# Kernel tuning notes

Hardware: AMD Instinct MI355X
Metric: run time of the kernel (lower is better)

## Reference

```python
import jax, jax.numpy as jnp
from jax import lax
import numpy as np

B, C, H, W = 8, 64, 56, 56
LM = 9              # level_map: NSCT subbands per channel
D = LM * C + C      # 640: swin block dim
DEPTH = 2
WIN = 7
HEADS = 8
KS = 5              # NSCT filter kernel size


def _nsct_filters():
    # fixed nonsubsampled 9-band filter bank (lowpass + 8 directional), stand-in for myNSCTd
    r = np.arange(KS) - KS // 2
    yy, xx = np.meshgrid(r, r, indexing='ij')
    g = np.exp(-(xx ** 2 + yy ** 2) / 4.0)
    g = g / g.sum()
    f = [g]
    for k in range(LM - 1):
        th = k * np.pi / (LM - 1)
        d = (np.cos(th) * xx + np.sin(th) * yy) * g
        d = d - d.mean()
        d = d / np.sqrt((d ** 2).sum())
        f.append(d)
    return jnp.asarray(np.stack(f), dtype=jnp.float32)  # [LM,KS,KS]


def _ct(x):
    # per-(b,c) NSCT decomposition -> [B, LM*C, H, W], band-major (matches transpose(0,2,1,3,4).reshape)
    Bx, Cx, Hx, Wx = x.shape
    K = _nsct_filters()
    k = jnp.tile(K, (Cx, 1, 1))[:, None]  # [Cx*LM,1,KS,KS], out channel index c*LM+band
    o = lax.conv_general_dilated(x, k, (1, 1), 'SAME',
                                 dimension_numbers=('NCHW', 'OIHW', 'NCHW'),
                                 feature_group_count=Cx)
    o = o.reshape(Bx, Cx, LM, Hx, Wx).transpose(0, 2, 1, 3, 4).reshape(Bx, LM * Cx, Hx, Wx)
    return o


def _ict(y):
    # inverse transform: reshape(B,LM,C,H,W).permute(0,2,1,3,4), reconstruct per channel
    Bx = y.shape[0]
    t = y.reshape(Bx, LM, C, H, W).transpose(0, 2, 1, 3, 4).reshape(Bx, C * LM, H, W)
    K = _nsct_filters()
    g = jnp.broadcast_to(K, (C, LM, KS, KS))  # groups=C: 9 subbands -> 1 channel each
    return lax.conv_general_dilated(t, g, (1, 1), 'SAME',
                                    dimension_numbers=('NCHW', 'OIHW', 'NCHW'),
                                    feature_group_count=C)


def _ln(x, g, b):
    m = x.mean(-1, keepdims=True)
    v = x.var(-1, keepdims=True)
    return (x - m) / jnp.sqrt(v + 1e-5) * g + b


def _attn_mask(shift):
    # standard SW-MSA mask for shifted windows
    img = np.zeros((H, W), np.int32)
    c = 0
    for hs in (slice(0, -WIN), slice(-WIN, -shift), slice(-shift, None)):
        for ws in (slice(0, -WIN), slice(-WIN, -shift), slice(-shift, None)):
            img[hs, ws] = c
            c += 1
    a = img.reshape(H // WIN, WIN, W // WIN, WIN).transpose(0, 2, 1, 3).reshape(-1, WIN * WIN)
    m = np.where(a[:, :, None] != a[:, None, :], -1e9, 0.0).astype(np.float32)
    return jnp.asarray(m)  # [nWindows, T, T]


def _swin_block(x, p, shift):
    Bx = x.shape[0]
    T = WIN * WIN
    dh = D // HEADS
    nH, nWw = H // WIN, W // WIN
    sc = x
    h = _ln(x, p['ln1_g'], p['ln1_b'])
    if shift:
        h = jnp.roll(h, (-shift, -shift), (1, 2))
    w = h.reshape(Bx, nH, WIN, nWw, WIN, D).transpose(0, 1, 3, 2, 4, 5).reshape(Bx * nH * nWw, T, D)
    qkv = w @ p['qkv_w'] + p['qkv_b']
    q, k, v = jnp.split(qkv, 3, axis=-1)
    heads = lambda t: t.reshape(-1, T, HEADS, dh).transpose(0, 2, 1, 3)
    q, k, v = heads(q), heads(k), heads(v)
    s = jnp.einsum('nhtd,nhsd->nhts', q, k) / jnp.sqrt(jnp.asarray(dh, x.dtype))
    if shift:
        m = _attn_mask(shift)
        s = (s.reshape(Bx, nH * nWw, HEADS, T, T) + m[None, :, None]).reshape(-1, HEADS, T, T)
    a = jax.nn.softmax(s, -1)
    o = jnp.einsum('nhts,nhsd->nhtd', a, v).transpose(0, 2, 1, 3).reshape(-1, T, D)
    o = o @ p['proj_w'] + p['proj_b']
    o = o.reshape(Bx, nH, nWw, WIN, WIN, D).transpose(0, 1, 3, 2, 4, 5).reshape(Bx, H, W, D)
    if shift:
        o = jnp.roll(o, (shift, shift), (1, 2))
    x = sc + o
    h2 = _ln(x, p['ln2_g'], p['ln2_b'])
    h2 = jax.nn.gelu(h2 @ p['fc1_w'] + p['fc1_b']) @ p['fc2_w'] + p['fc2_b']
    return x + h2


def setup_inputs() -> dict:
    key = jax.random.key(0)
    ks = jax.random.split(key, 8)
    s = 0.02
    n = lambda k, shp: jax.random.normal(k, shp, jnp.float32) * s
    return {
        'x': jax.random.normal(ks[0], (B, C, H, W), jnp.float32),
        'ln1_g': jnp.ones((DEPTH, D), jnp.float32), 'ln1_b': jnp.zeros((DEPTH, D), jnp.float32),
        'qkv_w': n(ks[1], (DEPTH, D, 3 * D)), 'qkv_b': jnp.zeros((DEPTH, 3 * D), jnp.float32),
        'proj_w': n(ks[2], (DEPTH, D, D)), 'proj_b': jnp.zeros((DEPTH, D), jnp.float32),
        'ln2_g': jnp.ones((DEPTH, D), jnp.float32), 'ln2_b': jnp.zeros((DEPTH, D), jnp.float32),
        'fc1_w': n(ks[3], (DEPTH, D, 4 * D)), 'fc1_b': jnp.zeros((DEPTH, 4 * D), jnp.float32),
        'fc2_w': n(ks[4], (DEPTH, 4 * D, D)), 'fc2_b': jnp.zeros((DEPTH, D), jnp.float32),
        'lin_w': n(ks[5], (D, LM * C)), 'lin_b': jnp.zeros((LM * C,), jnp.float32),
        'conv_w': n(ks[6], (C, D)), 'conv_b': jnp.zeros((C,), jnp.float32),
    }


def reference(x, ln1_g, ln1_b, qkv_w, qkv_b, proj_w, proj_b, ln2_g, ln2_b,
              fc1_w, fc1_b, fc2_w, fc2_b, lin_w, lin_b, conv_w, conv_b):
    x2 = jax.nn.relu(x)
    x_trans = lax.stop_gradient(_ct(x2))          # CT detaches its input in the original
    x3 = jnp.concatenate([x_trans, x2], axis=1)   # [B, 10C, H, W]
    x3 = x3.transpose(0, 2, 3, 1)                 # BHWC
    for i in range(DEPTH):
        p = dict(ln1_g=ln1_g[i], ln1_b=ln1_b[i], qkv_w=qkv_w[i], qkv_b=qkv_b[i],
                 proj_w=proj_w[i], proj_b=proj_b[i], ln2_g=ln2_g[i], ln2_b=ln2_b[i],
                 fc1_w=fc1_w[i], fc1_b=fc1_b[i], fc2_w=fc2_w[i], fc2_b=fc2_b[i])
        x3 = _swin_block(x3, p, 0 if i % 2 == 0 else WIN // 2)
    x3 = x3 @ lin_w + lin_b                        # D -> LM*C
    y = x3.transpose(0, 3, 1, 2)                   # [B, 9C, H, W]
    y_trans = lax.stop_gradient(_ict(y))           # ICT detaches its input in the original
    yc = jnp.concatenate([y_trans, y], axis=1)     # [B, 10C, H, W]
    out = jnp.einsum('bchw,oc->bohw', yc, conv_w) + conv_b[None, :, None, None]
    return out
```

## Files before the change

kernel.cpp:

```cpp
#include <hip/hip_runtime.h>
#include <hip/hip_bf16.h>
#include <math.h>

typedef __attribute__((ext_vector_type(4))) float f32x4;
typedef __attribute__((ext_vector_type(8))) short short8;

#define NTOK 25088
#define DD   640

__device__ __forceinline__ void gload_lds16(const void* g, void* l) {
    __builtin_amdgcn_global_load_lds((const __attribute__((address_space(1))) void*)g,
                                     (__attribute__((address_space(3))) void*)l,
                                     16, 0, 0);
}

__device__ __forceinline__ float gelu_f(float t) {
    float u = 1.5957691216057308f * (t + 0.044715f * t * t * t);
    float e = __builtin_amdgcn_exp2f(u * -1.4426950408889634f);
    return t / (1.f + e);
}

__global__ void init_consts(float* __restrict__ filt, float* __restrict__ linbp,
                            const float* __restrict__ lin_b, float* __restrict__ convbp,
                            const float* __restrict__ conv_b) {
    int t = threadIdx.x;
    if (t == 0) {
        float g[25]; float s = 0.f;
        for (int i = 0; i < 5; i++) for (int j = 0; j < 5; j++) {
            float yy = (float)(i - 2), xx = (float)(j - 2);
            float v = expf(-(xx*xx + yy*yy) * 0.25f);
            g[i*5+j] = v; s += v;
        }
        for (int i = 0; i < 25; i++) { g[i] /= s; filt[i] = g[i]; }
        for (int k = 0; k < 8; k++) {
            float th = (float)k * 3.14159265358979323846f / 8.f;
            float ct = cosf(th), st = sinf(th);
            float d[25]; float mean = 0.f;
            for (int i = 0; i < 5; i++) for (int j = 0; j < 5; j++) {
                float yy = (float)(i - 2), xx = (float)(j - 2);
                d[i*5+j] = (ct*xx + st*yy) * g[i*5+j];
                mean += d[i*5+j];
            }
            mean *= (1.f/25.f);
            float ss = 0.f;
            for (int i = 0; i < 25; i++) { d[i] -= mean; ss += d[i]*d[i]; }
            ss = sqrtf(ss);
            for (int i = 0; i < 25; i++) filt[(k+1)*25 + i] = d[i] / ss;
        }
    }
    for (int i = t; i < 640; i += 256) linbp[i]  = (i < 576) ? lin_b[i]  : 0.f;
    for (int i = t; i < 128; i += 256) convbp[i] = (i < 64)  ? conv_b[i] : 0.f;
}

__global__ __launch_bounds__(256)
void wtrans_kernel(const float* __restrict__ src, __hip_bfloat16* __restrict__ dst,
                   int K, int Nsrc) {
    __shared__ float tile[32][33];
    const int n0 = blockIdx.x * 32;
    const int k0 = blockIdx.y * 32;
    const int tx = threadIdx.x, ty = threadIdx.y;
    #pragma unroll
    for (int r = ty; r < 32; r += 8) {
        int k = k0 + r, n = n0 + tx;
        tile[r][tx] = (n < Nsrc) ? src[(long)k * Nsrc + n] : 0.f;
    }
    __syncthreads();
    #pragma unroll
    for (int r = ty; r < 32; r += 8) {
        int n = n0 + r, k = k0 + tx;
        dst[(long)n * K + k] = __float2bfloat16(tile[tx][r]);
    }
}

__global__ void wcast_kernel(const float* __restrict__ src, __hip_bfloat16* __restrict__ dst,
                             int count, int total) {
    int i = blockIdx.x * 256 + threadIdx.x;
    if (i < total) dst[i] = __float2bfloat16(i < count ? src[i] : 0.f);
}

__global__ __launch_bounds__(256)
void prep_kernel(const float* __restrict__ x, const float* __restrict__ filt,
                 float* __restrict__ x3) {
    __shared__ float sf[225];
    for (int i = threadIdx.x; i < 225; i += 256) sf[i] = filt[i];
    __syncthreads();
    int id = blockIdx.x * 256 + threadIdx.x;
    int c = id & 63;
    int pix = id >> 6;
    int w = pix % 56, h = (pix / 56) % 56, b = pix / 3136;
    const float* xp = x + (long)(b * 64 + c) * 3136;
    float nb[25];
    #pragma unroll
    for (int dy = 0; dy < 5; dy++) {
        int hy = h + dy - 2;
        #pragma unroll
        for (int dx = 0; dx < 5; dx++) {
            int wx = w + dx - 2;
            float v = 0.f;
            if (hy >= 0 && hy < 56 && wx >= 0 && wx < 56) v = fmaxf(xp[hy*56 + wx], 0.f);
            nb[dy*5 + dx] = v;
        }
    }
    float* orow = x3 + (long)pix * DD;
    #pragma unroll
    for (int band = 0; band < 9; band++) {
        float a = 0.f;
        #pragma unroll
        for (int t = 0; t < 25; t++) a += nb[t] * sf[band*25 + t];
        orow[band*64 + c] = a;
    }
    orow[576 + c] = nb[12];
}

__global__ __launch_bounds__(256)
void ln_kernel(const float* __restrict__ xin, const float* __restrict__ g,
               const float* __restrict__ bt, __hip_bfloat16* __restrict__ out) {
    const int lane = threadIdx.x & 63;
    const long tok = (long)blockIdx.x * 4 + (threadIdx.x >> 6);
    const float* xr = xin + tok * DD;
    float v[10]; float s = 0.f, s2 = 0.f;
    #pragma unroll
    for (int i = 0; i < 10; i++) { float t = xr[lane + (i << 6)]; v[i] = t; s += t; s2 += t*t; }
    #pragma unroll
    for (int o = 32; o > 0; o >>= 1) { s += __shfl_down(s, o); s2 += __shfl_down(s2, o); }
    s = __shfl(s, 0); s2 = __shfl(s2, 0);
    const float mean = s * (1.f/640.f);
    const float var  = s2 * (1.f/640.f) - mean * mean;
    const float inv  = 1.f / sqrtf(var + 1e-5f);
    __hip_bfloat16* orow = out + tok * DD;
    #pragma unroll
    for (int i = 0; i < 10; i++) {
        int c = lane + (i << 6);
        orow[c] = __float2bfloat16((v[i] - mean) * inv * g[c] + bt[c]);
    }
}

__global__ __launch_bounds__(256, 2)
void gemm128_kernel(const __hip_bfloat16* __restrict__ A,
                    const __hip_bfloat16* __restrict__ Bt,
                    const float* __restrict__ bias,
                    const float* __restrict__ resid,
                    float* __restrict__ Cf,
                    __hip_bfloat16* __restrict__ Cb,
                    int K, int ldc, int ncf, int ldb, int col_off, int ncb,
                    int act_gelu, int nvalid, int mode) {
    extern __shared__ __align__(16) char smraw[];
    __hip_bfloat16* sm = (__hip_bfloat16*)smraw;

    const int tid  = threadIdx.x;
    const int lane = tid & 63;
    const int wv   = tid >> 6;
    const int wr   = wv >> 1;
    const int wc   = wv & 1;

    const int gx   = gridDim.x;
    const int nwg  = gx * gridDim.y;
    const int orig = blockIdx.y * gx + blockIdx.x;
    const int qq = nwg >> 3, rr = nwg & 7;
    const int xcd = orig & 7, lid = orig >> 3;
    const int wg = (xcd < rr ? xcd * (qq + 1) : rr * (qq + 1) + (xcd - rr) * qq) + lid;
    const long m0 = (long)(wg / gx) * 128;
    const long n0 = (long)(wg % gx) * 128;

    const bool wact = ((int)n0 + (wc << 6)) < nvalid;

    f32x4 acc[4][4];
    #pragma unroll
    for (int i = 0; i < 4; i++)
        #pragma unroll
        for (int j = 0; j < 4; j++) acc[i][j] = (f32x4){0.f, 0.f, 0.f, 0.f};

    const int srow  = tid >> 3;
    const int slot  = tid & 7;
    const int sslot = slot ^ (srow & 7);
    const __hip_bfloat16* Agb = A  + (m0 + srow) * (long)K + (sslot << 3);
    const __hip_bfloat16* Bgb = Bt + (n0 + srow) * (long)K + (sslot << 3);
    __hip_bfloat16* dA = sm + srow * 64 + (slot << 3);
    __hip_bfloat16* dB = sm + 8192 + srow * 64 + (slot << 3);

    const int frow = lane & 15;
    const int fks  = lane >> 4;

    auto STAGE = [&](int b, int k0) {
        #pragma unroll
        for (int i = 0; i < 4; i++) {
            gload_lds16(Agb + (long)i * 32 * K + k0, dA + b * 16384 + i * 2048);
            gload_lds16(Bgb + (long)i * 32 * K + k0, dB + b * 16384 + i * 2048);
        }
    };

    const int nt = K >> 6;
    STAGE(0, 0);
    for (int t = 0; t < nt; ++t) {
        const int cur = t & 1;
        if (t + 1 < nt) {
            STAGE(cur ^ 1, (t + 1) << 6);
            asm volatile("s_waitcnt vmcnt(8)" ::: "memory");
        } else {
            asm volatile("s_waitcnt vmcnt(0)" ::: "memory");
        }
        __builtin_amdgcn_s_barrier();
        __builtin_amdgcn_sched_barrier(0);

        const __hip_bfloat16* pA = sm + cur * 16384;
        const __hip_bfloat16* pB = sm + 8192 + cur * 16384;
        if (wact) {
            #pragma unroll
            for (int ks = 0; ks < 2; ++ks) {
                short8 af[4], bfr[4];
                #pragma unroll
                for (int mi = 0; mi < 4; ++mi) {
                    const int R = (wr << 6) + (mi << 4) + frow;
                    af[mi] = *(const short8*)(pA + R * 64 + ((((ks << 2) | fks) ^ (R & 7)) << 3));
                }
                #pragma unroll
                for (int nj = 0; nj < 4; ++nj) {
                    const int Rn = (wc << 6) + (nj << 4) + frow;
                    bfr[nj] = *(const short8*)(pB + Rn * 64 + ((((ks << 2) | fks) ^ (Rn & 7)) << 3));
                }
                __builtin_amdgcn_s_setprio(1);
                #pragma unroll
                for (int mi = 0; mi < 4; ++mi)
                    #pragma unroll
                    for (int nj = 0; nj < 4; ++nj)
                        acc[mi][nj] = __builtin_amdgcn_mfma_f32_16x16x32_bf16(
                            bfr[nj], af[mi], acc[mi][nj], 0, 0, 0);
                __builtin_amdgcn_s_setprio(0);
            }
        }
        asm volatile("" ::: "memory");
        __builtin_amdgcn_s_barrier();
    }

    if (!wact) return;
    const int nlim = (ncf > ncb) ? ncf : ncb;
    #pragma unroll
    for (int mi = 0; mi < 4; ++mi) {
        const long row = m0 + (wr << 6) + (mi << 4) + frow;
        #pragma unroll
        for (int nj = 0; nj < 4; ++nj) {
            const int n = (int)n0 + (wc << 6) + (nj << 4) + (fks << 2);
            if (n >= nlim) continue;
            f32x4 v = acc[mi][nj];
            if (bias) {
                const f32x4 bv = *(const f32x4*)&bias[n];
                v += bv;
            }
            if (act_gelu) {
                v[0] = gelu_f(v[0]); v[1] = gelu_f(v[1]); v[2] = gelu_f(v[2]); v[3] = gelu_f(v[3]);
            }
            if (mode == 1) {
                const int b = (int)(row / 3136), pos = (int)(row % 3136);
                #pragma unroll
                for (int r = 0; r < 4; ++r)
                    Cf[(long)(b * 64 + n + r) * 3136 + pos] = v[r];
                continue;
            }
            if (resid && n < ncf) v += *(const f32x4*)&resid[row * (long)ldc + n];
            if (Cf && n < ncf) *(f32x4*)&Cf[row * (long)ldc + n] = v;
            if (Cb && n < ncb) {
                short4 p;
                p.x = (short)__bfloat16_as_short(__float2bfloat16(v[0]));
                p.y = (short)__bfloat16_as_short(__float2bfloat16(v[1]));
                p.z = (short)__bfloat16_as_short(__float2bfloat16(v[2]));
                p.w = (short)__bfloat16_as_short(__float2bfloat16(v[3]));
                *(short4*)&Cb[row * (long)ldb + col_off + n] = p;
            }
        }
    }
}

__global__ __launch_bounds__(256)
void attn_kernel(const __hip_bfloat16* __restrict__ qkv, __hip_bfloat16* __restrict__ o,
                 int shift) {
    __shared__ __align__(16) float qT[80][52];
    __shared__ __align__(16) float kT[80][52];
    __shared__ __align__(16) float vs[50][80];
    __shared__ __align__(16) float ss[49][52];
    __shared__ int toks[49];
    __shared__ int rid[49];

    const int tid = threadIdx.x;
    const int win = blockIdx.x >> 3;
    const int hd  = blockIdx.x & 7;
    const int b   = win >> 6;
    const int wh  = (win >> 3) & 7;
    const int ww  = win & 7;

    if (tid < 49) {
        int i = tid / 7, j = tid % 7;
        int ph = wh * 7 + i, pw = ww * 7 + j;
        int sh = ph + shift; if (sh >= 56) sh -= 56;
        int sw = pw + shift; if (sw >= 56) sw -= 56;
        toks[tid] = (b * 56 + sh) * 56 + sw;
        int rh = (ph < 49) ? 0 : ((ph < 53) ? 1 : 2);
        int rw = (pw < 49) ? 0 : ((pw < 53) ? 1 : 2);
        rid[tid] = rh * 3 + rw;
    }
    for (int i = tid; i < 80 * 3; i += 256) {
        int d = i / 3, cc = 49 + (i % 3);
        qT[d][cc] = 0.f; kT[d][cc] = 0.f;
    }
    __syncthreads();
    for (int idx = tid; idx < 49 * 80; idx += 256) {
        int t = idx / 80, d = idx % 80;
        long base = (long)toks[t] * 1920 + hd * 80 + d;
        qT[d][t] = __bfloat162float(qkv[base]);
        kT[d][t] = __bfloat162float(qkv[base + 640]);
        vs[t][d] = __bfloat162float(qkv[base + 1280]);
    }
    __syncthreads();
    const float scale = 0.11180339887498948f;
    for (int p = tid; p < 49 * 13; p += 256) {
        int t = p / 13, j0 = (p % 13) * 4;
        float4 a = {0.f, 0.f, 0.f, 0.f};
        #pragma unroll
        for (int d = 0; d < 80; d++) {
            float qv = qT[d][t];
            float4 kv = *(const float4*)&kT[d][j0];
            a.x += qv * kv.x; a.y += qv * kv.y; a.z += qv * kv.z; a.w += qv * kv.w;
        }
        a.x *= scale; a.y *= scale; a.z *= scale; a.w *= scale;
        *(float4*)&ss[t][j0] = a;
    }
    __syncthreads();
    if (tid < 49) {
        const int myr = rid[tid];
        float mx = -1e30f;
        for (int j = 0; j < 49; j++) {
            float v = ss[tid][j];
            if (shift && rid[j] != myr) v = -1e9f;
            ss[tid][j] = v;
            mx = fmaxf(mx, v);
        }
        float sum = 0.f;
        for (int j = 0; j < 49; j++) {
            float e = expf(ss[tid][j] - mx);
            ss[tid][j] = e; sum += e;
        }
        float inv = 1.f / sum;
        for (int j = 0; j < 49; j++) ss[tid][j] *= inv;
    }
    __syncthreads();
    for (int p = tid; p < 49 * 20; p += 256) {
        int t = p / 20, dv = (p % 20) * 4;
        float4 a = {0.f, 0.f, 0.f, 0.f};
        for (int j = 0; j < 49; j++) {
            float w = ss[t][j];
            float4 vv = *(const float4*)&vs[j][dv];
            a.x += w * vv.x; a.y += w * vv.y; a.z += w * vv.z; a.w += w * vv.w;
        }
        long base = (long)toks[t] * DD + hd * 80 + dv;
        o[base + 0] = __float2bfloat16(a.x);
        o[base + 1] = __float2bfloat16(a.y);
        o[base + 2] = __float2bfloat16(a.z);
        o[base + 3] = __float2bfloat16(a.w);
    }
}

__global__ __launch_bounds__(256)
void ict_kernel(const float* __restrict__ y, const float* __restrict__ filt,
                __hip_bfloat16* __restrict__ ayc) {
    __shared__ float sf[225];
    for (int i = threadIdx.x; i < 225; i += 256) sf[i] = filt[i];
    __syncthreads();
    int id = blockIdx.x * 256 + threadIdx.x;
    int c = id & 63;
    int pix = id >> 6;
    int w = pix % 56, h = (pix / 56) % 56, b = pix / 3136;
    float a = 0.f;
    #pragma unroll
    for (int dy = 0; dy < 5; dy++) {
        int hy = h + dy - 2;
        if (hy < 0 || hy >= 56) continue;
        #pragma unroll
        for (int dx = 0; dx < 5; dx++) {
            int wx = w + dx - 2;
            if (wx < 0 || wx >= 56) continue;
            const float* yr = y + ((long)(b * 56 + hy) * 56 + wx) * DD + c;
            #pragma unroll
            for (int band = 0; band < 9; band++)
                a += yr[band * 64] * sf[band*25 + dy*5 + dx];
        }
    }
    ayc[(long)pix * DD + c] = __float2bfloat16(a);
}

extern "C" void kernel_launch(void* const* d_in, const int* in_sizes, int n_in,
                              void* d_out, int out_size, void* d_ws, size_t ws_size,
                              hipStream_t stream) {
    (void)in_sizes; (void)n_in; (void)out_size; (void)ws_size;
    const float* x      = (const float*)d_in[0];
    const float* ln1_g  = (const float*)d_in[1];
    const float* ln1_b  = (const float*)d_in[2];
    const float* qkv_w  = (const float*)d_in[3];
    const float* qkv_b  = (const float*)d_in[4];
    const float* proj_w = (const float*)d_in[5];
    const float* proj_b = (const float*)d_in[6];
    const float* ln2_g  = (const float*)d_in[7];
    const float* ln2_b  = (const float*)d_in[8];
    const float* fc1_w  = (const float*)d_in[9];
    const float* fc1_b  = (const float*)d_in[10];
    const float* fc2_w  = (const float*)d_in[11];
    const float* fc2_b  = (const float*)d_in[12];
    const float* lin_w  = (const float*)d_in[13];
    const float* lin_b  = (const float*)d_in[14];
    const float* conv_w = (const float*)d_in[15];
    const float* conv_b = (const float*)d_in[16];

    char* ws = (char*)d_ws;
    size_t off = 0;
    auto alloc = [&](size_t bytes) -> void* {
        void* p = ws + off;
        off += (bytes + 255) & ~(size_t)255;
        return p;
    };
    float* filt   = (float*)alloc(225 * 4);
    float* linbp  = (float*)alloc(640 * 4);
    float* convbp = (float*)alloc(128 * 4);
    __hip_bfloat16* qkvWt[2], *projWt[2], *fc1Wt[2], *fc2Wt[2];
    for (int i = 0; i < 2; i++) qkvWt[i] = (__hip_bfloat16*)alloc(1920L * 640 * 2);
    for (int i = 0; i < 2; i++) projWt[i] = (__hip_bfloat16*)alloc(640L * 640 * 2);
    for (int i = 0; i < 2; i++) fc1Wt[i] = (__hip_bfloat16*)alloc(2560L * 640 * 2);
    for (int i = 0; i < 2; i++) fc2Wt[i] = (__hip_bfloat16*)alloc(640L * 2560 * 2);
    __hip_bfloat16* linWt  = (__hip_bfloat16*)alloc(640L * 640 * 2);
    __hip_bfloat16* convWt = (__hip_bfloat16*)alloc(128L * 640 * 2);
    float* x3 = (float*)alloc((long)NTOK * DD * 4);
    __hip_bfloat16* bufA = (__hip_bfloat16*)alloc((long)NTOK * DD * 2);
    char* bufB = (char*)alloc((long)NTOK * 2560 * 2);
    __hip_bfloat16* qkv = (__hip_bfloat16*)bufB;
    __hip_bfloat16* h2  = (__hip_bfloat16*)bufB;
    float* ybuf = (float*)bufB;
    __hip_bfloat16* ayc = (__hip_bfloat16*)(bufB + (long)NTOK * DD * 4);

    hipFuncSetAttribute((const void*)gemm128_kernel,
                        hipFuncAttributeMaxDynamicSharedMemorySize, 65536);

    dim3 tb(32, 8);
    init_consts<<<1, 256, 0, stream>>>(filt, linbp, lin_b, convbp, conv_b);
    for (int i = 0; i < 2; i++) {
        wtrans_kernel<<<dim3(60, 20), tb, 0, stream>>>(qkv_w + (long)i*640*1920, qkvWt[i], 640, 1920);
        wtrans_kernel<<<dim3(20, 20), tb, 0, stream>>>(proj_w + (long)i*640*640,  projWt[i], 640, 640);
        wtrans_kernel<<<dim3(80, 20), tb, 0, stream>>>(fc1_w + (long)i*640*2560, fc1Wt[i], 640, 2560);
        wtrans_kernel<<<dim3(20, 80), tb, 0, stream>>>(fc2_w + (long)i*2560*640, fc2Wt[i], 2560, 640);
    }
    wtrans_kernel<<<dim3(20, 20), tb, 0, stream>>>(lin_w, linWt, 640, 576);
    wcast_kernel<<<320, 256, 0, stream>>>(conv_w, convWt, 64 * 640, 128 * 640);

    prep_kernel<<<6272, 256, 0, stream>>>(x, filt, x3);

    for (int i = 0; i < 2; i++) {
        int shift = i ? 3 : 0;
        ln_kernel<<<6272, 256, 0, stream>>>(x3, ln1_g + i*640, ln1_b + i*640, bufA);
        gemm128_kernel<<<dim3(15, 196), 256, 65536, stream>>>(bufA, qkvWt[i], qkv_b + i*1920,
            nullptr, nullptr, qkv, 640, 0, 0, 1920, 0, 1920, 0, 1920, 0);
        attn_kernel<<<4096, 256, 0, stream>>>(qkv, bufA, shift);
        gemm128_kernel<<<dim3(5, 196), 256, 65536, stream>>>(bufA, projWt[i], proj_b + i*640,
            x3, x3, nullptr, 640, 640, 640, 0, 0, 0, 0, 640, 0);
        ln_kernel<<<6272, 256, 0, stream>>>(x3, ln2_g + i*640, ln2_b + i*640, bufA);
        gemm128_kernel<<<dim3(20, 196), 256, 65536, stream>>>(bufA, fc1Wt[i], fc1_b + i*2560,
            nullptr, nullptr, h2, 640, 0, 0, 2560, 0, 2560, 1, 2560, 0);
        gemm128_kernel<<<dim3(5, 196), 256, 65536, stream>>>(h2, fc2Wt[i], fc2_b + i*640,
            x3, x3, (i == 1) ? bufA : nullptr, 2560, 640, 640, 640, 0, (i == 1) ? 640 : 0, 0, 640, 0);
    }
    gemm128_kernel<<<dim3(5, 196), 256, 65536, stream>>>(bufA, linWt, linbp,
        nullptr, ybuf, ayc, 640, 640, 640, 640, 64, 576, 0, 576, 0);
    ict_kernel<<<6272, 256, 0, stream>>>(ybuf, filt, ayc);
    gemm128_kernel<<<dim3(1, 196), 256, 65536, stream>>>(ayc, convWt, convbp,
        nullptr, (float*)d_out, nullptr, 640, 0, 64, 0, 0, 0, 0, 64, 1);
}
```

Baseline: 1.489 ms.

## Pre-swizzle weights into MFMA fragment layout and stream B from global

Weights are repacked once into a per-lane MFMA fragment order, so each wave loads its B operand straight from global/L2 with one 16-byte load per lane and never stages it in LDS. The GEMM now stages only a 128x320 A chunk in LDS and assigns each wave a 64-column slice of a 128x256 output tile, with 8x4 accumulators per wave. This removes LDS traffic and barriers for B and doubles the N-tile width. The trade-offs are dependence on L2 bandwidth and latency for the weight loads, which are no longer double-buffered, heavier register pressure, and wasted columns where N is not a multiple of 256.

```diff
diff --git a/kernel.cpp b/kernel.cpp
--- a/kernel.cpp
+++ b/kernel.cpp
@@ -7,6 +7,8 @@
 
 #define NTOK 25088
 #define DD   640
+#define KC   320
+#define KSTEPS 10
 
 __device__ __forceinline__ void gload_lds16(const void* g, void* l) {
     __builtin_amdgcn_global_load_lds((const __attribute__((address_space(1))) void*)g,
@@ -53,29 +55,26 @@
 }
 
 __global__ __launch_bounds__(256)
-void wtrans_kernel(const float* __restrict__ src, __hip_bfloat16* __restrict__ dst,
-                   int K, int Nsrc) {
-    __shared__ float tile[32][33];
-    const int n0 = blockIdx.x * 32;
-    const int k0 = blockIdx.y * 32;
-    const int tx = threadIdx.x, ty = threadIdx.y;
-    #pragma unroll
-    for (int r = ty; r < 32; r += 8) {
-        int k = k0 + r, n = n0 + tx;
-        tile[r][tx] = (n < Nsrc) ? src[(long)k * Nsrc + n] : 0.f;
-    }
-    __syncthreads();
-    #pragma unroll
-    for (int r = ty; r < 32; r += 8) {
-        int n = n0 + r, k = k0 + tx;
-        dst[(long)n * K + k] = __float2bfloat16(tile[tx][r]);
-    }
-}
-
-__global__ void wcast_kernel(const float* __restrict__ src, __hip_bfloat16* __restrict__ dst,
-                             int count, int total) {
-    int i = blockIdx.x * 256 + threadIdx.x;
-    if (i < total) dst[i] = __float2bfloat16(i < count ? src[i] : 0.f);
+void wfrag_kernel(const float* __restrict__ src, __hip_bfloat16* __restrict__ dst,
+                  int K, int Nfrag, int Nsrc, int srcNK) {
+    int idx = blockIdx.x * 256 + threadIdx.x;
+    int total = (Nfrag >> 4) * (K >> 5) * 64;
+    if (idx >= total) return;
+    int lane = idx & 63;
+    int rest = idx >> 6;
+    int nk = K >> 5;
+    int kt = rest % nk;
+    int nt = rest / nk;
+    int n  = (nt << 4) + (lane & 15);
+    int k0 = (kt << 5) + ((lane >> 4) << 3);
+    short8 o;
+    #pragma unroll
+    for (int e = 0; e < 8; ++e) {
+        float v = 0.f;
+        if (n < Nsrc) v = srcNK ? src[(long)n * K + k0 + e] : src[(long)(k0 + e) * Nsrc + n];
+        o[e] = (short)__bfloat16_as_short(__float2bfloat16(v));
+    }
+    *((short8*)dst + idx) = o;
 }
 
 __global__ __launch_bounds__(256)
@@ -136,22 +135,19 @@
 }
 
 __global__ __launch_bounds__(256, 2)
-void gemm128_kernel(const __hip_bfloat16* __restrict__ A,
-                    const __hip_bfloat16* __restrict__ Bt,
-                    const float* __restrict__ bias,
-                    const float* __restrict__ resid,
-                    float* __restrict__ Cf,
-                    __hip_bfloat16* __restrict__ Cb,
-                    int K, int ldc, int ncf, int ldb, int col_off, int ncb,
-                    int act_gelu, int nvalid, int mode) {
+void gemmA_kernel(const __hip_bfloat16* __restrict__ A,
+                  const __hip_bfloat16* __restrict__ Wf,
+                  const float* __restrict__ bias,
+                  const float* __restrict__ resid,
+                  float* __restrict__ Cf,
+                  __hip_bfloat16* __restrict__ Cb,
+                  int K, int ldc, int ncf, int ldb, int col_off, int ncb,
+                  int act_gelu, int nvalid, int mode) {
     extern __shared__ __align__(16) char smraw[];
-    __hip_bfloat16* sm = (__hip_bfloat16*)smraw;
 
     const int tid  = threadIdx.x;
     const int lane = tid & 63;
     const int wv   = tid >> 6;
-    const int wr   = wv >> 1;
-    const int wc   = wv & 1;
 
     const int gx   = gridDim.x;
     const int nwg  = gx * gridDim.y;
@@ -160,92 +156,69 @@
     const int xcd = orig & 7, lid = orig >> 3;
     const int wg = (xcd < rr ? xcd * (qq + 1) : rr * (qq + 1) + (xcd - rr) * qq) + lid;
     const long m0 = (long)(wg / gx) * 128;
-    const long n0 = (long)(wg % gx) * 128;
-
-    const bool wact = ((int)n0 + (wc << 6)) < nvalid;
-
-    f32x4 acc[4][4];
-    #pragma unroll
-    for (int i = 0; i < 4; i++)
+    const int  n0w = (wg % gx) * 256 + (wv << 6);
+    const bool wact = n0w < nvalid;
+
+    f32x4 acc[8][4];
+    #pragma unroll
+    for (int i = 0; i < 8; i++)
         #pragma unroll
         for (int j = 0; j < 4; j++) acc[i][j] = (f32x4){0.f, 0.f, 0.f, 0.f};
-
-    const int srow  = tid >> 3;
-    const int slot  = tid & 7;
-    const int sslot = slot ^ (srow & 7);
-    const __hip_bfloat16* Agb = A  + (m0 + srow) * (long)K + (sslot << 3);
-    const __hip_bfloat16* Bgb = Bt + (n0 + srow) * (long)K + (sslot << 3);
-    __hip_bfloat16* dA = sm + srow * 64 + (slot << 3);
-    __hip_bfloat16* dB = sm + 8192 + srow * 64 + (slot << 3);
 
     const int frow = lane & 15;
     const int fks  = lane >> 4;
-
-    auto STAGE = [&](int b, int k0) {
-        #pragma unroll
-        for (int i = 0; i < 4; i++) {
-            gload_lds16(Agb + (long)i * 32 * K + k0, dA + b * 16384 + i * 2048);
-            gload_lds16(Bgb + (long)i * 32 * K + k0, dB + b * 16384 + i * 2048);
-        }
-    };
-
-    const int nt = K >> 6;
-    STAGE(0, 0);
-    for (int t = 0; t < nt; ++t) {
-        const int cur = t & 1;
-        if (t + 1 < nt) {
-            STAGE(cur ^ 1, (t + 1) << 6);
-            asm volatile("s_waitcnt vmcnt(8)" ::: "memory");
-        } else {
-            asm volatile("s_waitcnt vmcnt(0)" ::: "memory");
-        }
-        __builtin_amdgcn_s_barrier();
-        __builtin_amdgcn_sched_barrier(0);
-
-        const __hip_bfloat16* pA = sm + cur * 16384;
-        const __hip_bfloat16* pB = sm + 8192 + cur * 16384;
+    const int fr7  = frow & 7;
+    const int nkt  = K >> 5;
+    const int ntb  = n0w >> 4;
+
+    const int nchunks = K / KC;
+    for (int sc = 0; sc < nchunks; ++sc) {
+        if (sc) __syncthreads();
+        #pragma unroll
+        for (int j = 0; j < 20; ++j) {
+            const int ch = j * 256 + tid;
+            const int r  = ch / 40;
+            const int c  = ch - r * 40;
+            const int scs = (c & 0x38) | ((c ^ r) & 7);
+            gload_lds16(A + (m0 + r) * (long)K + sc * KC + scs * 8, smraw + ch * 16);
+        }
+        __syncthreads();
         if (wact) {
             #pragma unroll
-            for (int ks = 0; ks < 2; ++ks) {
-                short8 af[4], bfr[4];
+            for (int t = 0; t < KSTEPS; ++t) {
+                const int ksg = sc * KSTEPS + t;
+                short8 bq[4];
                 #pragma unroll
-                for (int mi = 0; mi < 4; ++mi) {
-                    const int R = (wr << 6) + (mi << 4) + frow;
-                    af[mi] = *(const short8*)(pA + R * 64 + ((((ks << 2) | fks) ^ (R & 7)) << 3));
-                }
+                for (int nj = 0; nj < 4; ++nj)
+                    bq[nj] = *((const short8*)Wf + ((long)(ntb + nj) * nkt + ksg) * 64 + lane);
+                short8 aq[8];
+                const int slot = ((((t << 2) | fks) ^ fr7) << 4);
                 #pragma unroll
-                for (int nj = 0; nj < 4; ++nj) {
-                    const int Rn = (wc << 6) + (nj << 4) + frow;
-                    bfr[nj] = *(const short8*)(pB + Rn * 64 + ((((ks << 2) | fks) ^ (Rn & 7)) << 3));
-                }
+                for (int mi = 0; mi < 8; ++mi)
+                    aq[mi] = *(const short8*)(smraw + ((mi << 4) + frow) * 640 + slot);
                 __builtin_amdgcn_s_setprio(1);
                 #pragma unroll
-                for (int mi = 0; mi < 4; ++mi)
+                for (int mi = 0; mi < 8; ++mi)
                     #pragma unroll
                     for (int nj = 0; nj < 4; ++nj)
                         acc[mi][nj] = __builtin_amdgcn_mfma_f32_16x16x32_bf16(
-                            bfr[nj], af[mi], acc[mi][nj], 0, 0, 0);
+                            bq[nj], aq[mi], acc[mi][nj], 0, 0, 0);
                 __builtin_amdgcn_s_setprio(0);
             }
         }
-        asm volatile("" ::: "memory");
-        __builtin_amdgcn_s_barrier();
     }
 
     if (!wact) return;
     const int nlim = (ncf > ncb) ? ncf : ncb;
     #pragma unroll
-    for (int mi = 0; mi < 4; ++mi) {
-        const long row = m0 + (wr << 6) + (mi << 4) + frow;
+    for (int mi = 0; mi < 8; ++mi) {
+        const long row = m0 + (mi << 4) + frow;
         #pragma unroll
         for (int nj = 0; nj < 4; ++nj) {
-            const int n = (int)n0 + (wc << 6) + (nj << 4) + (fks << 2);
+            const int n = n0w + (nj << 4) + (fks << 2);
             if (n >= nlim) continue;
             f32x4 v = acc[mi][nj];
-            if (bias) {
-                const f32x4 bv = *(const f32x4*)&bias[n];
-                v += bv;
-            }
+            if (bias) v += *(const f32x4*)&bias[n];
             if (act_gelu) {
                 v[0] = gelu_f(v[0]); v[1] = gelu_f(v[1]); v[2] = gelu_f(v[2]); v[3] = gelu_f(v[3]);
             }
@@ -418,13 +391,13 @@
     float* filt   = (float*)alloc(225 * 4);
     float* linbp  = (float*)alloc(640 * 4);
     float* convbp = (float*)alloc(128 * 4);
-    __hip_bfloat16* qkvWt[2], *projWt[2], *fc1Wt[2], *fc2Wt[2];
-    for (int i = 0; i < 2; i++) qkvWt[i] = (__hip_bfloat16*)alloc(1920L * 640 * 2);
-    for (int i = 0; i < 2; i++) projWt[i] = (__hip_bfloat16*)alloc(640L * 640 * 2);
-    for (int i = 0; i < 2; i++) fc1Wt[i] = (__hip_bfloat16*)alloc(2560L * 640 * 2);
-    for (int i = 0; i < 2; i++) fc2Wt[i] = (__hip_bfloat16*)alloc(640L * 2560 * 2);
-    __hip_bfloat16* linWt  = (__hip_bfloat16*)alloc(640L * 640 * 2);
-    __hip_bfloat16* convWt = (__hip_bfloat16*)alloc(128L * 640 * 2);
+    __hip_bfloat16* qkvWf[2], *projWf[2], *fc1Wf[2], *fc2Wf[2];
+    for (int i = 0; i < 2; i++) qkvWf[i] = (__hip_bfloat16*)alloc(1920L * 640 * 2);
+    for (int i = 0; i < 2; i++) projWf[i] = (__hip_bfloat16*)alloc(640L * 640 * 2);
+    for (int i = 0; i < 2; i++) fc1Wf[i] = (__hip_bfloat16*)alloc(2560L * 640 * 2);
+    for (int i = 0; i < 2; i++) fc2Wf[i] = (__hip_bfloat16*)alloc(640L * 2560 * 2);
+    __hip_bfloat16* linWf  = (__hip_bfloat16*)alloc(576L * 640 * 2);
+    __hip_bfloat16* convWf = (__hip_bfloat16*)alloc(64L * 640 * 2);
     float* x3 = (float*)alloc((long)NTOK * DD * 4);
     __hip_bfloat16* bufA = (__hip_bfloat16*)alloc((long)NTOK * DD * 2);
     char* bufB = (char*)alloc((long)NTOK * 2560 * 2);
@@ -433,39 +406,38 @@
     float* ybuf = (float*)bufB;
     __hip_bfloat16* ayc = (__hip_bfloat16*)(bufB + (long)NTOK * DD * 4);
 
-    hipFuncSetAttribute((const void*)gemm128_kernel,
-                        hipFuncAttributeMaxDynamicSharedMemorySize, 65536);
-
-    dim3 tb(32, 8);
+    hipFuncSetAttribute((const void*)gemmA_kernel,
+                        hipFuncAttributeMaxDynamicSharedMemorySize, 81920);
+
     init_consts<<<1, 256, 0, stream>>>(filt, linbp, lin_b, convbp, conv_b);
     for (int i = 0; i < 2; i++) {
-        wtrans_kernel<<<dim3(60, 20), tb, 0, stream>>>(qkv_w + (long)i*640*1920, qkvWt[i], 640, 1920);
-        wtrans_kernel<<<dim3(20, 20), tb, 0, stream>>>(proj_w + (long)i*640*640,  projWt[i], 640, 640);
-        wtrans_kernel<<<dim3(80, 20), tb, 0, stream>>>(fc1_w + (long)i*640*2560, fc1Wt[i], 640, 2560);
-        wtrans_kernel<<<dim3(20, 80), tb, 0, stream>>>(fc2_w + (long)i*2560*640, fc2Wt[i], 2560, 640);
-    }
-    wtrans_kernel<<<dim3(20, 20), tb, 0, stream>>>(lin_w, linWt, 640, 576);
-    wcast_kernel<<<320, 256, 0, stream>>>(conv_w, convWt, 64 * 640, 128 * 640);
+        wfrag_kernel<<<600, 256, 0, stream>>>(qkv_w + (long)i*640*1920, qkvWf[i], 640, 1920, 1920, 0);
+        wfrag_kernel<<<200, 256, 0, stream>>>(proj_w + (long)i*640*640,  projWf[i], 640, 640, 640, 0);
+        wfrag_kernel<<<800, 256, 0, stream>>>(fc1_w + (long)i*640*2560, fc1Wf[i], 640, 2560, 2560, 0);
+        wfrag_kernel<<<800, 256, 0, stream>>>(fc2_w + (long)i*2560*640, fc2Wf[i], 2560, 640, 640, 0);
+    }
+    wfrag_kernel<<<180, 256, 0, stream>>>(lin_w, linWf, 640, 576, 576, 0);
+    wfrag_kernel<<<20, 256, 0, stream>>>(conv_w, convWf, 640, 64, 64, 1);
 
     prep_kernel<<<6272, 256, 0, stream>>>(x, filt, x3);
 
     for (int i = 0; i < 2; i++) {
         int shift = i ? 3 : 0;
         ln_kernel<<<6272, 256, 0, stream>>>(x3, ln1_g + i*640, ln1_b + i*640, bufA);
-        gemm128_kernel<<<dim3(15, 196), 256, 65536, stream>>>(bufA, qkvWt[i], qkv_b + i*1920,
+        gemmA_kernel<<<dim3(8, 196), 256, 81920, stream>>>(bufA, qkvWf[i], qkv_b + i*1920,
             nullptr, nullptr, qkv, 640, 0, 0, 1920, 0, 1920, 0, 1920, 0);
         attn_kernel<<<4096, 256, 0, stream>>>(qkv, bufA, shift);
-        gemm128_kernel<<<dim3(5, 196), 256, 65536, stream>>>(bufA, projWt[i], proj_b + i*640,
+        gemmA_kernel<<<dim3(3, 196), 256, 81920, stream>>>(bufA, projWf[i], proj_b + i*640,
             x3, x3, nullptr, 640, 640, 640, 0, 0, 0, 0, 640, 0);
         ln_kernel<<<6272, 256, 0, stream>>>(x3, ln2_g + i*640, ln2_b + i*640, bufA);
-        gemm128_kernel<<<dim3(20, 196), 256, 65536, stream>>>(bufA, fc1Wt[i], fc1_b + i*2560,
+        gemmA_kernel<<<dim3(10, 196), 256, 81920, stream>>>(bufA, fc1Wf[i], fc1_b + i*2560,
             nullptr, nullptr, h2, 640, 0, 0, 2560, 0, 2560, 1, 2560, 0);
-        gemm128_kernel<<<dim3(5, 196), 256, 65536, stream>>>(h2, fc2Wt[i], fc2_b + i*640,
+        gemmA_kernel<<<dim3(3, 196), 256, 81920, stream>>>(h2, fc2Wf[i], fc2_b + i*640,
             x3, x3, (i == 1) ? bufA : nullptr, 2560, 640, 640, 640, 0, (i == 1) ? 640 : 0, 0, 640, 0);
     }
-    gemm128_kernel<<<dim3(5, 196), 256, 65536, stream>>>(bufA, linWt, linbp,
+    gemmA_kernel<<<dim3(3, 196), 256, 81920, stream>>>(bufA, linWf, linbp,
         nullptr, ybuf, ayc, 640, 640, 640, 640, 64, 576, 0, 576, 0);
     ict_kernel<<<6272, 256, 0, stream>>>(ybuf, filt, ayc);
-    gemm128_kernel<<<dim3(1, 196), 256, 65536, stream>>>(ayc, convWt, convbp,
+    gemmA_kernel<<<dim3(1, 196), 256, 81920, stream>>>(ayc, convWf, convbp,
         nullptr, (float*)d_out, nullptr, 640, 0, 64, 0, 0, 0, 0, 64, 1);
 }
```

After: 1.846 ms. 24.0% more time.
